# Kernel tuning notes

Measured on AMD Instinct MI355X. Metric: run time of the kernel, lower is better.

Reference implementation:

```python
import jax, jax.numpy as jnp
import numpy as np

N = 50000
E = 800000
IN_DIM = 128
HEADS = 4
OUT_DIM = 32
TOT = HEADS * OUT_DIM  # 128 == IN_DIM -> residual_proj is None
LN_EPS = 1e-5
NEG_SLOPE = 0.2


def setup_inputs() -> dict:
    key = jax.random.key(0)
    ks = jax.random.split(key, 10)
    x = jax.random.normal(ks[0], (N, IN_DIM), dtype=jnp.float32)
    # random edges guaranteed src != dst (PyG GATv2Conv removes then re-adds self loops)
    src = jax.random.randint(ks[1], (E,), 0, N)
    off = jax.random.randint(ks[2], (E,), 1, N)
    dst = (src + off) % N
    edge_index = jnp.stack([src, dst]).astype(jnp.int64)
    # glorot-style init for weights
    sc = 1.0 / np.sqrt(IN_DIM)
    W_l = jax.random.uniform(ks[3], (IN_DIM, TOT), jnp.float32, -sc, sc)
    b_l = jnp.zeros((TOT,), jnp.float32)
    W_r = jax.random.uniform(ks[4], (IN_DIM, TOT), jnp.float32, -sc, sc)
    b_r = jnp.zeros((TOT,), jnp.float32)
    att = jax.random.uniform(ks[5], (HEADS, OUT_DIM), jnp.float32, -sc, sc)
    bias = jnp.zeros((TOT,), jnp.float32)
    ln_g = jnp.ones((TOT,), jnp.float32)
    ln_b = jnp.zeros((TOT,), jnp.float32)
    return {"x": x, "edge_index": edge_index, "W_l": W_l, "b_l": b_l,
            "W_r": W_r, "b_r": b_r, "att": att, "bias": bias,
            "ln_g": ln_g, "ln_b": ln_b}


def _gatv2_layer(x, src, dst, W_l, b_l, W_r, b_r, att, bias, ln_g, ln_b):
    n = x.shape[0]
    # GATv2Conv: x_l = lin_l(x) (source/messages), x_r = lin_r(x) (target)
    xl = (x @ W_l + b_l).reshape(n, HEADS, OUT_DIM)
    xr = (x @ W_r + b_r).reshape(n, HEADS, OUT_DIM)
    m = xl[src] + xr[dst]                               # [E+N, H, D]
    s = jnp.einsum('ehd,hd->eh', jax.nn.leaky_relu(m, NEG_SLOPE), att)
    # per-destination softmax (every node has a self loop -> no empty segments)
    smax = jax.ops.segment_max(s, dst, num_segments=n)  # [N, H]
    e = jnp.exp(s - smax[dst])
    denom = jax.ops.segment_sum(e, dst, num_segments=n)
    alpha = e / denom[dst]                              # [E+N, H]
    out = jax.ops.segment_sum(alpha[..., None] * xl[src], dst, num_segments=n)
    out = out.reshape(n, TOT) + bias
    out = out + x                                       # residual (in_dim == total_out_dim)
    mu = jnp.mean(out, axis=-1, keepdims=True)
    var = jnp.mean(jnp.square(out - mu), axis=-1, keepdims=True)
    y = (out - mu) / jnp.sqrt(var + LN_EPS) * ln_g + ln_b
    return jax.nn.elu(y)


def reference(x, edge_index, W_l, b_l, W_r, b_r, att, bias, ln_g, ln_b):
    n = x.shape[0]
    loops = jnp.arange(n, dtype=edge_index.dtype)
    src = jnp.concatenate([edge_index[0], loops])
    dst = jnp.concatenate([edge_index[1], loops])
    return _gatv2_layer(x, src, dst, W_l, b_l, W_r, b_r, att, bias, ln_g, ln_b)
```

## Files before the change

### kernel.cpp

```cpp
#include <hip/hip_runtime.h>

#define N_NODES 50000
#define E_EDGES 800000
#define M_TOTAL (E_EDGES + N_NODES)
#define IN_DIM 128
#define HEADS 4
#define OUT_DIM 32
#define TOT 128
#define LN_EPS 1e-5f
#define NEG_SLOPE 0.2f

#define SCAN_NBLK ((N_NODES + 255) / 256)
#define GEMM_NBLK ((N_NODES + 63) / 64)
#define CHUNK_NBLK ((M_TOTAL / 4 + 255) / 256)
#define ZERO_NBLK ((8 * N_NODES / 4 + 255) / 256)

typedef __bf16 bf16x8 __attribute__((ext_vector_type(8)));
typedef float  f32x4  __attribute__((ext_vector_type(4)));
typedef _Float16 h2   __attribute__((ext_vector_type(2)));

__device__ __forceinline__ float quad_sum(float p) {
    p += __int_as_float(__builtin_amdgcn_update_dpp(
        0, __float_as_int(p), 0xB1 , 0xF, 0xF, true));
    p += __int_as_float(__builtin_amdgcn_update_dpp(
        0, __float_as_int(p), 0x4E , 0xF, 0xF, true));
    return p;
}

__global__ __launch_bounds__(256) void init_kernel(
    const float* __restrict__ Wl, const float* __restrict__ Wr,
    unsigned* __restrict__ WT, int* __restrict__ deg8) {
    const int b = blockIdx.x, t = threadIdx.x;
    if (b < 64) {
        const int u = b * 256 + t;
        const int col = u >> 6, k2 = u & 63;
        const float* __restrict__ W = (col < 128) ? Wl : Wr;
        const int c = col & 127;
        union { __bf16 bb[2]; unsigned uu; } p;
        p.bb[0] = (__bf16)W[(2 * k2) * TOT + c];
        p.bb[1] = (__bf16)W[(2 * k2 + 1) * TOT + c];
        WT[col * 64 + k2] = p.uu;
    } else {
        const int i = (b - 64) * 256 + t;
        if (i < 8 * N_NODES / 4) ((int4*)deg8)[i] = make_int4(0, 0, 0, 0);
    }
}

__global__ __launch_bounds__(256) void histgemm_kernel(
    const int* __restrict__ dsts, int* __restrict__ deg8,
    unsigned char* __restrict__ rank8,
    const float* __restrict__ x, const unsigned* __restrict__ WT,
    const float* __restrict__ bl, const float* __restrict__ br,
    unsigned* __restrict__ xlb, unsigned* __restrict__ xrb) {
    if (blockIdx.x >= GEMM_NBLK) {
        const int hb = blockIdx.x - GEMM_NBLK;
        const int m0 = (hb * 256 + threadIdx.x) * 4;
        if (m0 >= M_TOTAL) return;
        int d[4];
        if (m0 < E_EDGES) {
            const int4 dv = *(const int4*)&dsts[m0];
            d[0] = dv.x; d[1] = dv.y; d[2] = dv.z; d[3] = dv.w;
        } else {
            d[0] = m0 - E_EDGES; d[1] = d[0] + 1; d[2] = d[0] + 2; d[3] = d[0] + 3;
        }
        const int shard = (m0 >> 8) & 7;
        int* __restrict__ cnt = deg8 + shard * N_NODES;
        uchar4 r;
        r.x = (unsigned char)atomicAdd(&cnt[d[0]], 1);
        r.y = (unsigned char)atomicAdd(&cnt[d[1]], 1);
        r.z = (unsigned char)atomicAdd(&cnt[d[2]], 1);
        r.w = (unsigned char)atomicAdd(&cnt[d[3]], 1);
        *(uchar4*)&rank8[m0] = r;
        return;
    }
    __shared__ float epi[4][16][66];
    const int t = threadIdx.x, w = t >> 6, lane = t & 63;
    const int q = lane >> 4, ln = lane & 15;
    const int m0 = blockIdx.x * 64;

    const int row = min(m0 + w * 16 + ln, N_NODES - 1);
    const float* __restrict__ xrow = x + (size_t)row * IN_DIM;
    bf16x8 A[4];
#pragma unroll
    for (int c = 0; c < 4; ++c) {
        const float4 v0 = *(const float4*)&xrow[c * 32 + q * 8];
        const float4 v1 = *(const float4*)&xrow[c * 32 + q * 8 + 4];
        bf16x8 a;
        a[0] = (__bf16)v0.x; a[1] = (__bf16)v0.y; a[2] = (__bf16)v0.z; a[3] = (__bf16)v0.w;
        a[4] = (__bf16)v1.x; a[5] = (__bf16)v1.y; a[6] = (__bf16)v1.z; a[7] = (__bf16)v1.w;
        A[c] = a;
    }

    const int mr = lane >> 2, cg2 = (lane & 3) * 16;
    const int grow = m0 + w * 16 + mr;
#pragma unroll
    for (int g = 0; g < 4; ++g) {
        const int n0 = g * 64;
        const float* __restrict__ bvec = (g < 2) ? bl : br;
        f32x4 acc[4];
#pragma unroll
        for (int nt = 0; nt < 4; ++nt) {
            const float b = bvec[(n0 & 127) + nt * 16 + ln];
            acc[nt] = (f32x4){b, b, b, b};
        }
#pragma unroll
        for (int nt = 0; nt < 4; ++nt) {
            const int col = n0 + nt * 16 + ln;
#pragma unroll
            for (int c = 0; c < 4; ++c) {
                const bf16x8 B = *(const bf16x8*)&WT[col * 64 + c * 16 + q * 4];
                acc[nt] = __builtin_amdgcn_mfma_f32_16x16x32_bf16(A[c], B, acc[nt], 0, 0, 0);
            }
        }
#pragma unroll
        for (int nt = 0; nt < 4; ++nt)
#pragma unroll
            for (int r = 0; r < 4; ++r)
                epi[w][q * 4 + r][nt * 16 + ln] = acc[nt][r];

        if (grow < N_NODES) {
            unsigned p[8];
#pragma unroll
            for (int i = 0; i < 8; ++i) {
                union { _Float16 h[2]; unsigned u; } pk;
                pk.h[0] = (_Float16)epi[w][mr][cg2 + 2 * i];
                pk.h[1] = (_Float16)epi[w][mr][cg2 + 2 * i + 1];
                p[i] = pk.u;
            }
            unsigned* __restrict__ dst = ((g < 2) ? xlb : xrb) +
                (size_t)grow * 64 + (g & 1) * 32 + (cg2 >> 1);
            *(uint4*)&dst[0] = make_uint4(p[0], p[1], p[2], p[3]);
            *(uint4*)&dst[4] = make_uint4(p[4], p[5], p[6], p[7]);
        }
    }
}

__global__ __launch_bounds__(256) void scan1_kernel(
    const int* __restrict__ deg8, unsigned char* __restrict__ base8,
    int* __restrict__ incl, int* __restrict__ blockSums,
    int* __restrict__ degtot) {
    __shared__ int sh[256];
    const int t = threadIdx.x;
    const int i = blockIdx.x * 256 + t;
    int tot = 0;
    if (i < N_NODES) {
        int run = 0;
#pragma unroll
        for (int s = 0; s < 8; ++s) {
            base8[s * N_NODES + i] = (unsigned char)run;
            run += deg8[s * N_NODES + i];
        }
        tot = run;
        degtot[i] = tot;
    }
    sh[t] = tot;
    __syncthreads();
#pragma unroll
    for (int off = 1; off < 256; off <<= 1) {
        int u = (t >= off) ? sh[t - off] : 0;
        __syncthreads();
        sh[t] += u;
        __syncthreads();
    }
    if (i < N_NODES) incl[i] = sh[t];
    if (t == 255) blockSums[blockIdx.x] = sh[255];
}

__global__ __launch_bounds__(256) void scan23_kernel(
    const int* __restrict__ degtot, const int* __restrict__ blockSums,
    int* __restrict__ rowptr ) {
    __shared__ int sh[256];
    const int t = threadIdx.x;
    const int v0 = (t < SCAN_NBLK) ? blockSums[t] : 0;
    sh[t] = v0;
    __syncthreads();
#pragma unroll
    for (int off = 1; off < 256; off <<= 1) {
        int u = (t >= off) ? sh[t - off] : 0;
        __syncthreads();
        sh[t] += u;
        __syncthreads();
    }
    const int blockOff = (blockIdx.x == 0) ? 0 : sh[blockIdx.x - 1];
    const int i = blockIdx.x * 256 + t;
    if (i < N_NODES)
        rowptr[i] = blockOff + rowptr[i] - degtot[i];
    if (i == 0) rowptr[N_NODES] = M_TOTAL;
}

__global__ __launch_bounds__(256) void scatter_kernel(
    const int* __restrict__ srcs, const int* __restrict__ dsts,
    const int* __restrict__ rowptr, const unsigned char* __restrict__ base8,
    const unsigned char* __restrict__ rank8,
    unsigned short* __restrict__ sorted16) {
    const int m0 = (blockIdx.x * 256 + threadIdx.x) * 4;
    if (m0 >= M_TOTAL) return;
    int s[4], d[4];
    if (m0 < E_EDGES) {
        const int4 sv = *(const int4*)&srcs[m0];
        const int4 dv = *(const int4*)&dsts[m0];
        s[0] = sv.x; s[1] = sv.y; s[2] = sv.z; s[3] = sv.w;
        d[0] = dv.x; d[1] = dv.y; d[2] = dv.z; d[3] = dv.w;
    } else {
        s[0] = d[0] = m0 - E_EDGES;
        s[1] = d[1] = d[0] + 1; s[2] = d[2] = d[0] + 2; s[3] = d[3] = d[0] + 3;
    }
    const int shard = (m0 >> 8) & 7;
    const unsigned char* __restrict__ bs = base8 + shard * N_NODES;
    const uchar4 r = *(const uchar4*)&rank8[m0];
    const int p0 = rowptr[d[0]] + (int)bs[d[0]] + (int)r.x;
    const int p1 = rowptr[d[1]] + (int)bs[d[1]] + (int)r.y;
    const int p2 = rowptr[d[2]] + (int)bs[d[2]] + (int)r.z;
    const int p3 = rowptr[d[3]] + (int)bs[d[3]] + (int)r.w;
    sorted16[p0] = (unsigned short)s[0];
    sorted16[p1] = (unsigned short)s[1];
    sorted16[p2] = (unsigned short)s[2];
    sorted16[p3] = (unsigned short)s[3];
}

__global__ __launch_bounds__(256) void gat_kernel(
    const int* __restrict__ rowptr, const unsigned short* __restrict__ sorted16,
    const unsigned* __restrict__ xlb, const unsigned* __restrict__ xrb,
    const float* __restrict__ att, const float* __restrict__ x,
    const float* __restrict__ bias, const float* __restrict__ g,
    const float* __restrict__ bvec, float* __restrict__ out) {
    const int d = blockIdx.x * 4 + (threadIdx.x >> 6);
    const int lane = threadIdx.x & 63;
    const int ln = lane & 15, q = lane >> 4;
    if (d >= N_NODES) return;

    h2 xrh[4], ath[4];
    {
        const uint4 ur = *(const uint4*)&xrb[(size_t)d * 64 + 4 * ln];
        union { uint4 u; h2 h[4]; } cr; cr.u = ur;
        xrh[0] = cr.h[0]; xrh[1] = cr.h[1]; xrh[2] = cr.h[2]; xrh[3] = cr.h[3];
        const float4 a0 = *(const float4*)&att[8 * ln];
        const float4 a1 = *(const float4*)&att[8 * ln + 4];
        ath[0][0] = (_Float16)a0.x; ath[0][1] = (_Float16)a0.y;
        ath[1][0] = (_Float16)a0.z; ath[1][1] = (_Float16)a0.w;
        ath[2][0] = (_Float16)a1.x; ath[2][1] = (_Float16)a1.y;
        ath[3][0] = (_Float16)a1.z; ath[3][1] = (_Float16)a1.w;
    }
    const h2 slope = (h2){(_Float16)NEG_SLOPE, (_Float16)NEG_SLOPE};
    const int beg = rowptr[d], end = rowptr[d + 1];

    float l = 0.f;
    h2 acc4[4];
#pragma unroll
    for (int k = 0; k < 4; ++k) acc4[k] = (h2){(_Float16)0.f, (_Float16)0.f};

    int s_b = (int)sorted16[min(beg + 4 + q, end - 1)];
    uint4 u;
    {
        const int s_a = (int)sorted16[min(beg + q, end - 1)];
        u = *(const uint4*)&xlb[(size_t)s_a * 64 + 4 * ln];
    }

    for (int base = beg; base < end; base += 4) {
        const int s_c = (int)sorted16[min(base + 8 + q, end - 1)];
        const uint4 u_next = *(const uint4*)&xlb[(size_t)s_b * 64 + 4 * ln];

        const bool valid = (base + q) < end;
        union { unsigned uu; h2 h; } c0, c1, c2, c3;
        c0.uu = u.x; c1.uu = u.y; c2.uu = u.z; c3.uu = u.w;
        h2 m0 = c0.h + xrh[0], m1 = c1.h + xrh[1];
        h2 m2 = c2.h + xrh[2], m3 = c3.h + xrh[3];
        m0 = __builtin_elementwise_max(m0, m0 * slope);
        m1 = __builtin_elementwise_max(m1, m1 * slope);
        m2 = __builtin_elementwise_max(m2, m2 * slope);
        m3 = __builtin_elementwise_max(m3, m3 * slope);
        float p = __builtin_amdgcn_fdot2(m0, ath[0], 0.0f, false);
        p = __builtin_amdgcn_fdot2(m1, ath[1], p, false);
        p = __builtin_amdgcn_fdot2(m2, ath[2], p, false);
        p = __builtin_amdgcn_fdot2(m3, ath[3], p, false);
        p = quad_sum(p);
        const float e = valid ? __expf(p) : 0.f;
        l += e;
        const _Float16 eh = (_Float16)e;
        const h2 e2 = (h2){eh, eh};
        acc4[0] += e2 * c0.h;
        acc4[1] += e2 * c1.h;
        acc4[2] += e2 * c2.h;
        acc4[3] += e2 * c3.h;

        u = u_next; s_b = s_c;
    }

#pragma unroll
    for (int off = 16; off <= 32; off <<= 1) {
        l += __shfl_xor(l, off, 64);
#pragma unroll
        for (int k = 0; k < 4; ++k) {
            union { h2 h; int i; } tmp; tmp.h = acc4[k];
            tmp.i = __shfl_xor(tmp.i, off, 64);
            acc4[k] += tmp.h;
        }
    }
    float acc[8];
#pragma unroll
    for (int k = 0; k < 4; ++k) {
        acc[2 * k]     = (float)acc4[k][0];
        acc[2 * k + 1] = (float)acc4[k][1];
    }

    const float inv_l = 1.0f / l;
    const float4 xv0 = *(const float4*)&x[(size_t)d * TOT + 8 * ln];
    const float4 xv1 = *(const float4*)&x[(size_t)d * TOT + 8 * ln + 4];
    const float4 bi0 = *(const float4*)&bias[8 * ln];
    const float4 bi1 = *(const float4*)&bias[8 * ln + 4];
    float v[8];
    v[0] = fmaf(acc[0], inv_l, bi0.x + xv0.x);
    v[1] = fmaf(acc[1], inv_l, bi0.y + xv0.y);
    v[2] = fmaf(acc[2], inv_l, bi0.z + xv0.z);
    v[3] = fmaf(acc[3], inv_l, bi0.w + xv0.w);
    v[4] = fmaf(acc[4], inv_l, bi1.x + xv1.x);
    v[5] = fmaf(acc[5], inv_l, bi1.y + xv1.y);
    v[6] = fmaf(acc[6], inv_l, bi1.z + xv1.z);
    v[7] = fmaf(acc[7], inv_l, bi1.w + xv1.w);
    float sum = 0.f, sq = 0.f;
#pragma unroll
    for (int k = 0; k < 8; ++k) { sum += v[k]; sq = fmaf(v[k], v[k], sq); }
#pragma unroll
    for (int off = 1; off <= 8; off <<= 1) {
        sum += __shfl_xor(sum, off, 64);
        sq  += __shfl_xor(sq,  off, 64);
    }
    const float mu  = sum * (1.0f / TOT);
    const float var = sq * (1.0f / TOT) - mu * mu;
    const float inv = rsqrtf(var + LN_EPS);
    const float4 g0 = *(const float4*)&g[8 * ln];
    const float4 g1 = *(const float4*)&g[8 * ln + 4];
    const float4 b0 = *(const float4*)&bvec[8 * ln];
    const float4 b1 = *(const float4*)&bvec[8 * ln + 4];
    float y[8];
    y[0] = (v[0] - mu) * inv * g0.x + b0.x;
    y[1] = (v[1] - mu) * inv * g0.y + b0.y;
    y[2] = (v[2] - mu) * inv * g0.z + b0.z;
    y[3] = (v[3] - mu) * inv * g0.w + b0.w;
    y[4] = (v[4] - mu) * inv * g1.x + b1.x;
    y[5] = (v[5] - mu) * inv * g1.y + b1.y;
    y[6] = (v[6] - mu) * inv * g1.z + b1.z;
    y[7] = (v[7] - mu) * inv * g1.w + b1.w;
#pragma unroll
    for (int k = 0; k < 8; ++k) y[k] = y[k] > 0.f ? y[k] : __expf(y[k]) - 1.f;
    if (q < 2) {
        float4 o = (q == 0) ? make_float4(y[0], y[1], y[2], y[3])
                            : make_float4(y[4], y[5], y[6], y[7]);
        *(float4*)&out[(size_t)d * TOT + 8 * ln + 4 * q] = o;
    }
}

extern "C" void kernel_launch(void* const* d_in, const int* in_sizes, int n_in,
                              void* d_out, int out_size, void* d_ws, size_t ws_size,
                              hipStream_t stream) {
    const float* x    = (const float*)d_in[0];
    const int*   ei   = (const int*)d_in[1];
    const float* Wl   = (const float*)d_in[2];
    const float* bl   = (const float*)d_in[3];
    const float* Wr   = (const float*)d_in[4];
    const float* br   = (const float*)d_in[5];
    const float* att  = (const float*)d_in[6];
    const float* bias = (const float*)d_in[7];
    const float* ln_g = (const float*)d_in[8];
    const float* ln_b = (const float*)d_in[9];
    const int* srcs = ei;
    const int* dsts = ei + E_EDGES;

    unsigned* xlb = (unsigned*)d_ws;
    unsigned* xrb = xlb + (size_t)N_NODES * 64;
    int*   deg8       = (int*)(xrb + (size_t)N_NODES * 64);
    int*   degtot     = deg8 + 8 * N_NODES;
    int*   rowptr     = degtot + N_NODES;
    int*   blockSums  = rowptr + N_NODES + 1;
    unsigned* WT      = (unsigned*)(blockSums + SCAN_NBLK);
    unsigned short* sorted16 = (unsigned short*)(WT + 256 * 64);
    unsigned char*  base8    = (unsigned char*)(sorted16 + M_TOTAL);
    unsigned char*  rank8    = base8 + 8 * N_NODES;

    init_kernel<<<64 + ZERO_NBLK, 256, 0, stream>>>(Wl, Wr, WT, deg8);
    histgemm_kernel<<<GEMM_NBLK + CHUNK_NBLK, 256, 0, stream>>>(
        dsts, deg8, rank8, x, WT, bl, br, xlb, xrb);
    scan1_kernel<<<SCAN_NBLK, 256, 0, stream>>>(deg8, base8, rowptr, blockSums, degtot);
    scan23_kernel<<<SCAN_NBLK, 256, 0, stream>>>(degtot, blockSums, rowptr);
    scatter_kernel<<<CHUNK_NBLK, 256, 0, stream>>>(srcs, dsts, rowptr, base8, rank8, sorted16);
    gat_kernel<<<(N_NODES + 3) / 4, 256, 0, stream>>>(rowptr, sorted16, xlb, xrb, att, x,
                                                      bias, ln_g, ln_b, (float*)d_out);
}
```

Before: 206.0 us.

## Replace global-atomic degree histogram with LDS-private per-block histograms

Degree counting and rank assignment now run in 64 blocks, each using a shared-memory histogram of packed 16-bit counters over half the node range per pass. This replaces the earlier 8-shard global atomics and the zeroing pass. The per-block byte counts are prefix-summed across the 64 histograms in scan1. The GEMM moves to run alongside the scatter kernel instead of the histogram. This is meant to cut contended global atomics and one launch, at the cost of each block rereading its edge chunk twice and scan1 reading 64 histogram rows per node.

```diff
diff --git a/kernel.cpp b/kernel.cpp
--- a/kernel.cpp
+++ b/kernel.cpp
@@ -13,7 +13,9 @@
 #define SCAN_NBLK ((N_NODES + 255) / 256)
 #define GEMM_NBLK ((N_NODES + 63) / 64)
 #define CHUNK_NBLK ((M_TOTAL / 4 + 255) / 256)
-#define ZERO_NBLK ((8 * N_NODES / 4 + 255) / 256)
+#define HIST_NBLK 64
+#define EPB 13312
+#define HALF 25000
 
 typedef __bf16 bf16x8 __attribute__((ext_vector_type(8)));
 typedef float  f32x4  __attribute__((ext_vector_type(4)));
@@ -27,9 +29,12 @@
     return p;
 }
 
-__global__ __launch_bounds__(256) void init_kernel(
+__global__ __launch_bounds__(256) void wthist_kernel(
+    const int* __restrict__ dsts,
     const float* __restrict__ Wl, const float* __restrict__ Wr,
-    unsigned* __restrict__ WT, int* __restrict__ deg8) {
+    unsigned* __restrict__ WT, unsigned char* __restrict__ H,
+    unsigned char* __restrict__ rank8) {
+    __shared__ unsigned cnt[HALF / 2];
     const int b = blockIdx.x, t = threadIdx.x;
     if (b < 64) {
         const int u = b * 256 + t;
@@ -40,37 +45,127 @@
         p.bb[0] = (__bf16)W[(2 * k2) * TOT + c];
         p.bb[1] = (__bf16)W[(2 * k2 + 1) * TOT + c];
         WT[col * 64 + k2] = p.uu;
-    } else {
-        const int i = (b - 64) * 256 + t;
-        if (i < 8 * N_NODES / 4) ((int4*)deg8)[i] = make_int4(0, 0, 0, 0);
-    }
-}
-
-__global__ __launch_bounds__(256) void histgemm_kernel(
-    const int* __restrict__ dsts, int* __restrict__ deg8,
-    unsigned char* __restrict__ rank8,
+        return;
+    }
+    const int hb = b - 64;
+    const int m_begin = hb * EPB;
+    const int m_end = min(m_begin + EPB, M_TOTAL);
+    for (int pass = 0; pass < 2; ++pass) {
+        const int lo = pass * HALF;
+        for (int i = t; i < HALF / 2; i += 256) cnt[i] = 0;
+        __syncthreads();
+        for (int m0 = m_begin + t * 4; m0 < m_end; m0 += 1024) {
+            int d[4];
+            if (m0 < E_EDGES) {
+                const int4 dv = *(const int4*)&dsts[m0];
+                d[0] = dv.x; d[1] = dv.y; d[2] = dv.z; d[3] = dv.w;
+            } else {
+                d[0] = m0 - E_EDGES; d[1] = d[0] + 1; d[2] = d[0] + 2; d[3] = d[0] + 3;
+            }
+#pragma unroll
+            for (int k = 0; k < 4; ++k) {
+                const int dd = d[k] - lo;
+                if ((unsigned)dd < (unsigned)HALF) {
+                    const int sh = (dd & 1) * 16;
+                    const unsigned old = atomicAdd(&cnt[dd >> 1], 1u << sh);
+                    rank8[m0 + k] = (unsigned char)((old >> sh) & 0xffffu);
+                }
+            }
+        }
+        __syncthreads();
+        unsigned* __restrict__ Hrow = (unsigned*)(H + (size_t)hb * N_NODES + lo);
+        for (int i = t; i < HALF / 4; i += 256) {
+            const unsigned w0 = cnt[2 * i], w1 = cnt[2 * i + 1];
+            Hrow[i] = (w0 & 0xffu) | (((w0 >> 16) & 0xffu) << 8) |
+                      ((w1 & 0xffu) << 16) | (((w1 >> 16) & 0xffu) << 24);
+        }
+        __syncthreads();
+    }
+}
+
+__global__ __launch_bounds__(256) void scan1_kernel(
+    const unsigned char* __restrict__ H, unsigned char* __restrict__ P,
+    int* __restrict__ incl, int* __restrict__ blockSums,
+    int* __restrict__ degtot) {
+    __shared__ int sh[256];
+    const int t = threadIdx.x;
+    const int i = blockIdx.x * 256 + t;
+    int tot = 0;
+    if (i < N_NODES) {
+        int run = 0;
+#pragma unroll
+        for (int b = 0; b < HIST_NBLK; ++b) {
+            const int h = H[(size_t)b * N_NODES + i];
+            P[(size_t)b * N_NODES + i] = (unsigned char)run;
+            run += h;
+        }
+        tot = run;
+        degtot[i] = tot;
+    }
+    sh[t] = tot;
+    __syncthreads();
+#pragma unroll
+    for (int off = 1; off < 256; off <<= 1) {
+        int u = (t >= off) ? sh[t - off] : 0;
+        __syncthreads();
+        sh[t] += u;
+        __syncthreads();
+    }
+    if (i < N_NODES) incl[i] = sh[t];
+    if (t == 255) blockSums[blockIdx.x] = sh[255];
+}
+
+__global__ __launch_bounds__(256) void scan23_kernel(
+    const int* __restrict__ degtot, const int* __restrict__ blockSums,
+    int* __restrict__ rowptr ) {
+    __shared__ int sh[256];
+    const int t = threadIdx.x;
+    const int v0 = (t < SCAN_NBLK) ? blockSums[t] : 0;
+    sh[t] = v0;
+    __syncthreads();
+#pragma unroll
+    for (int off = 1; off < 256; off <<= 1) {
+        int u = (t >= off) ? sh[t - off] : 0;
+        __syncthreads();
+        sh[t] += u;
+        __syncthreads();
+    }
+    const int blockOff = (blockIdx.x == 0) ? 0 : sh[blockIdx.x - 1];
+    const int i = blockIdx.x * 256 + t;
+    if (i < N_NODES)
+        rowptr[i] = blockOff + rowptr[i] - degtot[i];
+    if (i == 0) rowptr[N_NODES] = M_TOTAL;
+}
+
+__global__ __launch_bounds__(256) void scattergemm_kernel(
+    const int* __restrict__ srcs, const int* __restrict__ dsts,
+    const int* __restrict__ rowptr, const unsigned char* __restrict__ P,
+    const unsigned char* __restrict__ rank8,
+    unsigned short* __restrict__ sorted16,
     const float* __restrict__ x, const unsigned* __restrict__ WT,
     const float* __restrict__ bl, const float* __restrict__ br,
     unsigned* __restrict__ xlb, unsigned* __restrict__ xrb) {
     if (blockIdx.x >= GEMM_NBLK) {
-        const int hb = blockIdx.x - GEMM_NBLK;
-        const int m0 = (hb * 256 + threadIdx.x) * 4;
+        const int sb = blockIdx.x - GEMM_NBLK;
+        const int m0 = (sb * 256 + threadIdx.x) * 4;
         if (m0 >= M_TOTAL) return;
-        int d[4];
+        int s[4], d[4];
         if (m0 < E_EDGES) {
+            const int4 sv = *(const int4*)&srcs[m0];
             const int4 dv = *(const int4*)&dsts[m0];
+            s[0] = sv.x; s[1] = sv.y; s[2] = sv.z; s[3] = sv.w;
             d[0] = dv.x; d[1] = dv.y; d[2] = dv.z; d[3] = dv.w;
         } else {
-            d[0] = m0 - E_EDGES; d[1] = d[0] + 1; d[2] = d[0] + 2; d[3] = d[0] + 3;
-        }
-        const int shard = (m0 >> 8) & 7;
-        int* __restrict__ cnt = deg8 + shard * N_NODES;
-        uchar4 r;
-        r.x = (unsigned char)atomicAdd(&cnt[d[0]], 1);
-        r.y = (unsigned char)atomicAdd(&cnt[d[1]], 1);
-        r.z = (unsigned char)atomicAdd(&cnt[d[2]], 1);
-        r.w = (unsigned char)atomicAdd(&cnt[d[3]], 1);
-        *(uchar4*)&rank8[m0] = r;
+            s[0] = d[0] = m0 - E_EDGES;
+            s[1] = d[1] = d[0] + 1; s[2] = d[2] = d[0] + 2; s[3] = d[3] = d[0] + 3;
+        }
+        const int hb = m0 / EPB;
+        const unsigned char* __restrict__ Pb = P + (size_t)hb * N_NODES;
+        const uchar4 r = *(const uchar4*)&rank8[m0];
+        sorted16[rowptr[d[0]] + (int)Pb[d[0]] + (int)r.x] = (unsigned short)s[0];
+        sorted16[rowptr[d[1]] + (int)Pb[d[1]] + (int)r.y] = (unsigned short)s[1];
+        sorted16[rowptr[d[2]] + (int)Pb[d[2]] + (int)r.z] = (unsigned short)s[2];
+        sorted16[rowptr[d[3]] + (int)Pb[d[3]] + (int)r.w] = (unsigned short)s[3];
         return;
     }
     __shared__ float epi[4][16][66];
@@ -133,89 +228,6 @@
             *(uint4*)&dst[4] = make_uint4(p[4], p[5], p[6], p[7]);
         }
     }
-}
-
-__global__ __launch_bounds__(256) void scan1_kernel(
-    const int* __restrict__ deg8, unsigned char* __restrict__ base8,
-    int* __restrict__ incl, int* __restrict__ blockSums,
-    int* __restrict__ degtot) {
-    __shared__ int sh[256];
-    const int t = threadIdx.x;
-    const int i = blockIdx.x * 256 + t;
-    int tot = 0;
-    if (i < N_NODES) {
-        int run = 0;
-#pragma unroll
-        for (int s = 0; s < 8; ++s) {
-            base8[s * N_NODES + i] = (unsigned char)run;
-            run += deg8[s * N_NODES + i];
-        }
-        tot = run;
-        degtot[i] = tot;
-    }
-    sh[t] = tot;
-    __syncthreads();
-#pragma unroll
-    for (int off = 1; off < 256; off <<= 1) {
-        int u = (t >= off) ? sh[t - off] : 0;
-        __syncthreads();
-        sh[t] += u;
-        __syncthreads();
-    }
-    if (i < N_NODES) incl[i] = sh[t];
-    if (t == 255) blockSums[blockIdx.x] = sh[255];
-}
-
-__global__ __launch_bounds__(256) void scan23_kernel(
-    const int* __restrict__ degtot, const int* __restrict__ blockSums,
-    int* __restrict__ rowptr ) {
-    __shared__ int sh[256];
-    const int t = threadIdx.x;
-    const int v0 = (t < SCAN_NBLK) ? blockSums[t] : 0;
-    sh[t] = v0;
-    __syncthreads();
-#pragma unroll
-    for (int off = 1; off < 256; off <<= 1) {
-        int u = (t >= off) ? sh[t - off] : 0;
-        __syncthreads();
-        sh[t] += u;
-        __syncthreads();
-    }
-    const int blockOff = (blockIdx.x == 0) ? 0 : sh[blockIdx.x - 1];
-    const int i = blockIdx.x * 256 + t;
-    if (i < N_NODES)
-        rowptr[i] = blockOff + rowptr[i] - degtot[i];
-    if (i == 0) rowptr[N_NODES] = M_TOTAL;
-}
-
-__global__ __launch_bounds__(256) void scatter_kernel(
-    const int* __restrict__ srcs, const int* __restrict__ dsts,
-    const int* __restrict__ rowptr, const unsigned char* __restrict__ base8,
-    const unsigned char* __restrict__ rank8,
-    unsigned short* __restrict__ sorted16) {
-    const int m0 = (blockIdx.x * 256 + threadIdx.x) * 4;
-    if (m0 >= M_TOTAL) return;
-    int s[4], d[4];
-    if (m0 < E_EDGES) {
-        const int4 sv = *(const int4*)&srcs[m0];
-        const int4 dv = *(const int4*)&dsts[m0];
-        s[0] = sv.x; s[1] = sv.y; s[2] = sv.z; s[3] = sv.w;
-        d[0] = dv.x; d[1] = dv.y; d[2] = dv.z; d[3] = dv.w;
-    } else {
-        s[0] = d[0] = m0 - E_EDGES;
-        s[1] = d[1] = d[0] + 1; s[2] = d[2] = d[0] + 2; s[3] = d[3] = d[0] + 3;
-    }
-    const int shard = (m0 >> 8) & 7;
-    const unsigned char* __restrict__ bs = base8 + shard * N_NODES;
-    const uchar4 r = *(const uchar4*)&rank8[m0];
-    const int p0 = rowptr[d[0]] + (int)bs[d[0]] + (int)r.x;
-    const int p1 = rowptr[d[1]] + (int)bs[d[1]] + (int)r.y;
-    const int p2 = rowptr[d[2]] + (int)bs[d[2]] + (int)r.z;
-    const int p3 = rowptr[d[3]] + (int)bs[d[3]] + (int)r.w;
-    sorted16[p0] = (unsigned short)s[0];
-    sorted16[p1] = (unsigned short)s[1];
-    sorted16[p2] = (unsigned short)s[2];
-    sorted16[p3] = (unsigned short)s[3];
 }
 
 __global__ __launch_bounds__(256) void gat_kernel(
@@ -368,21 +380,20 @@
 
     unsigned* xlb = (unsigned*)d_ws;
     unsigned* xrb = xlb + (size_t)N_NODES * 64;
-    int*   deg8       = (int*)(xrb + (size_t)N_NODES * 64);
-    int*   degtot     = deg8 + 8 * N_NODES;
+    int*   degtot     = (int*)(xrb + (size_t)N_NODES * 64);
     int*   rowptr     = degtot + N_NODES;
     int*   blockSums  = rowptr + N_NODES + 1;
-    unsigned* WT      = (unsigned*)(blockSums + SCAN_NBLK);
-    unsigned short* sorted16 = (unsigned short*)(WT + 256 * 64);
-    unsigned char*  base8    = (unsigned char*)(sorted16 + M_TOTAL);
-    unsigned char*  rank8    = base8 + 8 * N_NODES;
-
-    init_kernel<<<64 + ZERO_NBLK, 256, 0, stream>>>(Wl, Wr, WT, deg8);
-    histgemm_kernel<<<GEMM_NBLK + CHUNK_NBLK, 256, 0, stream>>>(
-        dsts, deg8, rank8, x, WT, bl, br, xlb, xrb);
-    scan1_kernel<<<SCAN_NBLK, 256, 0, stream>>>(deg8, base8, rowptr, blockSums, degtot);
+    unsigned* WT      = (unsigned*)(blockSums + SCAN_NBLK + 3);
+    unsigned char* H  = (unsigned char*)(WT + 256 * 64);
+    unsigned char* P  = H + (size_t)HIST_NBLK * N_NODES;
+    unsigned short* sorted16 = (unsigned short*)(P + (size_t)HIST_NBLK * N_NODES);
+    unsigned char*  rank8    = (unsigned char*)(sorted16 + M_TOTAL);
+
+    wthist_kernel<<<64 + HIST_NBLK, 256, 0, stream>>>(dsts, Wl, Wr, WT, H, rank8);
+    scan1_kernel<<<SCAN_NBLK, 256, 0, stream>>>(H, P, rowptr, blockSums, degtot);
     scan23_kernel<<<SCAN_NBLK, 256, 0, stream>>>(degtot, blockSums, rowptr);
-    scatter_kernel<<<CHUNK_NBLK, 256, 0, stream>>>(srcs, dsts, rowptr, base8, rank8, sorted16);
+    scattergemm_kernel<<<GEMM_NBLK + CHUNK_NBLK, 256, 0, stream>>>(
+        srcs, dsts, rowptr, P, rank8, sorted16, x, WT, bl, br, xlb, xrb);
     gat_kernel<<<(N_NODES + 3) / 4, 256, 0, stream>>>(rowptr, sorted16, xlb, xrb, att, x,
                                                       bias, ln_g, ln_b, (float*)d_out);
 }
```

Result: faster. 195.5 us (-5.1%).
